# Kernel optimization log

Measured on AMD Instinct MI355X. Metric: run time of the kernel, lower is better.

The kernel has to match this reference:

```python
import jax, jax.numpy as jnp
import numpy as np

B, N, C, H, D = 1, 4096, 256, 8, 64  # batch, seq, channels, heads, head_dim


def setup_inputs() -> dict:
    key = jax.random.key(0)
    ks = jax.random.split(key, 11)
    s = 0.02
    return {
        "q_x": jax.random.normal(ks[0], (B, N, C), jnp.float32),
        "k_x": jax.random.normal(ks[1], (B, N, C), jnp.float32),
        "v_x": jax.random.normal(ks[2], (B, N, C), jnp.float32),
        "bias": jax.random.normal(ks[3], (B, 1, N, N), jnp.float32),
        "wq": jax.random.normal(ks[4], (H * D, C), jnp.float32) * s,
        "wk": jax.random.normal(ks[5], (H * D, C), jnp.float32) * s,
        "wv": jax.random.normal(ks[6], (H * D, C), jnp.float32) * s,
        "wg": jax.random.normal(ks[7], (H * D, C), jnp.float32) * s,
        "bg": jnp.ones((H * D,), jnp.float32),  # gating bias init = 1
        "wo": jax.random.normal(ks[8], (C, H * D), jnp.float32) * s,
        "bo": jnp.zeros((C,), jnp.float32),
        "q_chunk_size": 256,
        "kv_chunk_size": 1024,
    }


def reference(q_x, k_x, v_x, bias, wq, wk, wv, wg, bg, wo, bo,
              q_chunk_size, kv_chunk_size):
    # The chunked Rabe-Staats loop computes exact softmax attention; the
    # chunk sizes are memory knobs only, so the reference computes the
    # mathematically identical full attention.
    q = (q_x @ wq.T).reshape(*q_x.shape[:-1], H, D) / jnp.sqrt(jnp.asarray(D, q_x.dtype))
    k = (k_x @ wk.T).reshape(*k_x.shape[:-1], H, D)
    v = (v_x @ wv.T).reshape(*v_x.shape[:-1], H, D)
    logits = jnp.einsum("bqhd,bkhd->bhqk", q, k) + bias  # [B,H,Q,K]
    p = jax.nn.softmax(logits, axis=-1)
    o = jnp.einsum("bkhd,bhqk->bqhd", v, p)  # [B,Q,H,D]
    g = jax.nn.sigmoid(q_x @ wg.T + bg).reshape(*q_x.shape[:-1], H, D)
    o = o * g
    o = o.reshape(*o.shape[:-2], H * D)
    return o @ wo.T + bo
```

## Files before the change

kernel.cpp:

```cpp
#include <hip/hip_runtime.h>
#include <stdint.h>

#define NN 4096
#define CC 256
#define HD 512
#define DD 64
#define KSPLIT 3

typedef __attribute__((ext_vector_type(8))) short short8;
typedef __attribute__((ext_vector_type(4))) float floatx4;

__device__ __forceinline__ unsigned short f2bf(float x) {
    union { float f; unsigned int u; } v; v.f = x;
    unsigned int u = v.u + 0x7fffu + ((v.u >> 16) & 1u);
    return (unsigned short)(u >> 16);
}
__device__ __forceinline__ float bf2f(unsigned short s) {
    union { unsigned int u; float f; } v; v.u = ((unsigned int)s) << 16;
    return v.f;
}

#if defined(__has_builtin) && __has_builtin(__builtin_amdgcn_cvt_pk_bf16_f32)
typedef __attribute__((ext_vector_type(2))) __bf16 bf16x2_t;
__device__ __forceinline__ unsigned int pack2bf(float a, float b) {
    union { bf16x2_t v; unsigned int u; } x;
    x.v = __builtin_amdgcn_cvt_pk_bf16_f32(a, b);
    return x.u;
}
#else
__device__ __forceinline__ unsigned int pack2bf(float a, float b) {
    return ((unsigned int)f2bf(b) << 16) | (unsigned int)f2bf(a);
}
#endif

#define GLOAD_LDS(gp, lp) __builtin_amdgcn_global_load_lds(                    \
    (__attribute__((address_space(1))) void*)(gp),                             \
    (__attribute__((address_space(3))) void*)(lp), 16, 0, 0)

__global__ __launch_bounds__(256) void prep_kernel(
    const float* __restrict__ qx, const float* __restrict__ kx,
    const float* __restrict__ vx,
    const float* __restrict__ wq, const float* __restrict__ wk,
    const float* __restrict__ wv, const float* __restrict__ wg,
    const float* __restrict__ wo,
    unsigned short* __restrict__ qxb, unsigned short* __restrict__ kxb,
    unsigned short* __restrict__ vxb, unsigned short* __restrict__ Wb,
    unsigned short* __restrict__ wob)
{
    const int z = blockIdx.y;
    const float* src; unsigned short* dst; int n; float s = 1.0f;
    switch (z) {
        case 0: src = qx; dst = qxb; n = NN * CC; break;
        case 1: src = kx; dst = kxb; n = NN * CC; break;
        case 2: src = vx; dst = vxb; n = NN * CC; break;
        case 3: src = wq; dst = Wb;               n = HD * CC; s = 0.125f; break;
        case 4: src = wk; dst = Wb + 1 * HD * CC; n = HD * CC; break;
        case 5: src = wv; dst = Wb + 2 * HD * CC; n = HD * CC; break;
        case 6: src = wg; dst = Wb + 3 * HD * CC; n = HD * CC; break;
        default: src = wo; dst = wob;             n = CC * HD; break;
    }
    int i = (blockIdx.x * 256 + threadIdx.x) * 4;
    if (i < n) {
        float4 v = *(const float4*)&src[i];
        ushort4 p;
        p.x = f2bf(v.x * s); p.y = f2bf(v.y * s);
        p.z = f2bf(v.z * s); p.w = f2bf(v.w * s);
        *(ushort4*)&dst[i] = p;
    }
}

__global__ __launch_bounds__(256, 8) void proj_kernel(
    const unsigned short* __restrict__ qxb, const unsigned short* __restrict__ kxb,
    const unsigned short* __restrict__ vxb, const unsigned short* __restrict__ Wb,
    const float* __restrict__ bg,
    unsigned short* __restrict__ Qb, unsigned short* __restrict__ Kb,
    unsigned short* __restrict__ VbT, unsigned short* __restrict__ Gb)
{
    const int m0 = blockIdx.x * 64;
    const int nb = blockIdx.y;
    const int mode = nb >> 3;
    const int subn = nb & 7;
    const int n0 = mode * HD + subn * 64;
    const unsigned short* X = (mode == 1) ? kxb : (mode == 2) ? vxb : qxb;

    const int tid = threadIdx.x;
    const int wid = tid >> 6;
    const int lane = tid & 63;
    const int quad = lane >> 4;
    const int ln = lane & 15;
    const int lnx = ln & 7;

    __shared__ __align__(16) unsigned short smem[2 * 64 * 64];
    unsigned short* Xs = smem;
    unsigned short* Ws = smem + 64 * 64;

    floatx4 acc[4] = {};

    for (int k0 = 0; k0 < CC; k0 += 64) {
        #pragma unroll
        for (int t = 0; t < 2; t++) {
            int row = wid * 16 + t * 8 + (lane >> 3);
            int c = (lane & 7) ^ (lane >> 3);
            GLOAD_LDS(&X[(size_t)(m0 + row) * CC + k0 + c * 8],
                      &Xs[(wid * 16 + t * 8) * 64]);
            GLOAD_LDS(&Wb[(size_t)(n0 + row) * CC + k0 + c * 8],
                      &Ws[(wid * 16 + t * 8) * 64]);
        }
        __syncthreads();

        #pragma unroll
        for (int ks = 0; ks < 64; ks += 32) {
            const int cb = ks >> 3;
            short8 a = *(const short8*)&Xs[(wid * 16 + ln) * 64 +
                                           (((quad ^ cb) ^ lnx) * 8)];
            #pragma unroll
            for (int n = 0; n < 4; n++) {
                short8 b = *(const short8*)&Ws[(n * 16 + ln) * 64 +
                                               (((quad ^ cb) ^ lnx) * 8)];
                acc[n] = __builtin_amdgcn_mfma_f32_16x16x32_bf16(a, b, acc[n], 0, 0, 0);
            }
        }
        __syncthreads();
    }

    if (mode != 2) {
        unsigned short* Out = (mode == 0) ? Qb : (mode == 1) ? Kb : Gb;
        #pragma unroll
        for (int n = 0; n < 4; n++) {
            int col = subn * 64 + n * 16 + ln;
            float bgv = (mode == 3) ? bg[col] : 0.0f;
            #pragma unroll
            for (int r = 0; r < 4; r++) {
                int row = m0 + wid * 16 + quad * 4 + r;
                float v = acc[n][r];
                if (mode == 3) v = 1.0f / (1.0f + __expf(-(v + bgv)));
                Out[(size_t)row * HD + col] = f2bf(v);
            }
        }
    } else {
        #pragma unroll
        for (int n = 0; n < 4; n++) {
            int cl = n * 16 + ln;
            #pragma unroll
            for (int r = 0; r < 4; r++) {
                int rl = wid * 16 + quad * 4 + r;
                smem[cl * 72 + rl] = f2bf(acc[n][r]);
            }
        }
        __syncthreads();
        #pragma unroll
        for (int it = 0; it < 2; it++) {
            int idx = it * 256 + tid;
            int c = idx >> 3, ch = idx & 7;
            short8 vv = *(const short8*)&smem[c * 72 + ch * 8];
            *(short8*)&VbT[(size_t)(subn * 64 + c) * NN + m0 + ch * 8] = vv;
        }
    }
}

__global__ __launch_bounds__(256, 6) void attn_kernel(
    const unsigned short* __restrict__ Qb, const unsigned short* __restrict__ Kb,
    const unsigned short* __restrict__ VbT,
    const float* __restrict__ bias,
    unsigned short* __restrict__ Opart, float* __restrict__ Lpart)
{
    const int h = blockIdx.y;
    const int q0 = blockIdx.x * 64;
    const int sp = blockIdx.z;
    const int tbeg = (sp * 64) / KSPLIT;
    const int tend = ((sp + 1) * 64) / KSPLIT;
    const int tid = threadIdx.x;
    const int wid = tid >> 6;
    const int lane = tid & 63;
    const int quad = lane >> 4;
    const int ln = lane & 15;
    const int lnx = ln & 7;

    __shared__ __align__(16) unsigned short Ks[64 * 64];
    __shared__ __align__(16) unsigned short Vs[64 * 64];
    __shared__ __align__(16) unsigned short Ps[64 * 72];

    const int qrow = q0 + wid * 16 + ln;
    short8 qa0 = *(const short8*)&Qb[(size_t)qrow * HD + h * DD + quad * 8];
    short8 qa1 = *(const short8*)&Qb[(size_t)qrow * HD + h * DD + 32 + quad * 8];

    floatx4 O[4] = {};
    float lsum[4] = {0.0f, 0.0f, 0.0f, 0.0f};

    for (int kt = tbeg; kt < tend; kt++) {
        const int k0 = kt * 64;
        #pragma unroll
        for (int t = 0; t < 2; t++) {
            int row = wid * 16 + t * 8 + (lane >> 3);
            int c = (lane & 7) ^ (lane >> 3);
            GLOAD_LDS(&Kb[(size_t)(k0 + row) * HD + h * DD + c * 8],
                      &Ks[(wid * 16 + t * 8) * 64]);
            GLOAD_LDS(&VbT[(size_t)(h * DD + row) * NN + k0 + c * 8],
                      &Vs[(wid * 16 + t * 8) * 64]);
        }

        float bv[4][4];
        #pragma unroll
        for (int r = 0; r < 4; r++) {
            const float* brow = &bias[(size_t)(q0 + wid * 16 + quad * 4 + r) * NN + k0];
            #pragma unroll
            for (int n = 0; n < 4; n++) bv[r][n] = brow[n * 16 + ln];
        }
        __syncthreads();

        floatx4 S[4];
        #pragma unroll
        for (int n = 0; n < 4; n++)
            S[n] = (floatx4){bv[0][n], bv[1][n], bv[2][n], bv[3][n]};
        #pragma unroll
        for (int n = 0; n < 4; n++) {
            short8 b0 = *(const short8*)&Ks[(n * 16 + ln) * 64 + ((quad ^ lnx) * 8)];
            S[n] = __builtin_amdgcn_mfma_f32_16x16x32_bf16(qa0, b0, S[n], 0, 0, 0);
            short8 b1 = *(const short8*)&Ks[(n * 16 + ln) * 64 + (((quad ^ 4) ^ lnx) * 8)];
            S[n] = __builtin_amdgcn_mfma_f32_16x16x32_bf16(qa1, b1, S[n], 0, 0, 0);
        }

        #pragma unroll
        for (int r = 0; r < 4; r++) {
            int prow = (wid * 16 + quad * 4 + r) * 72;
            #pragma unroll
            for (int n = 0; n < 4; n += 2) {
                float p0 = __expf(S[n][r]);
                float p1 = __expf(S[n + 1][r]);
                lsum[r] += p0 + p1;
                unsigned int pk = pack2bf(p0, p1);
                Ps[prow + n * 16 + ln] = (unsigned short)(pk & 0xffffu);
                Ps[prow + (n + 1) * 16 + ln] = (unsigned short)(pk >> 16);
            }
        }

        #pragma unroll
        for (int ks = 0; ks < 64; ks += 32) {
            const int cb = ks >> 3;
            short8 a = *(const short8*)&Ps[(wid * 16 + ln) * 72 + ks + quad * 8];
            #pragma unroll
            for (int nd = 0; nd < 4; nd++) {
                short8 b = *(const short8*)&Vs[(nd * 16 + ln) * 64 +
                                               (((quad ^ cb) ^ lnx) * 8)];
                O[nd] = __builtin_amdgcn_mfma_f32_16x16x32_bf16(a, b, O[nd], 0, 0, 0);
            }
        }
        __syncthreads();
    }

    #pragma unroll
    for (int r = 0; r < 4; r++) {
        #pragma unroll
        for (int off = 1; off < 16; off <<= 1)
            lsum[r] += __shfl_xor(lsum[r], off);
        int grow = q0 + wid * 16 + quad * 4 + r;
        size_t base = ((size_t)(sp * 8 + h) * NN + grow) * 64;
        #pragma unroll
        for (int nd = 0; nd < 4; nd++)
            Opart[base + nd * 16 + ln] = f2bf(O[nd][r]);
        if (ln == 0)
            Lpart[(size_t)(sp * 8 + h) * NN + grow] = lsum[r];
    }
}

__global__ __launch_bounds__(256) void combine_kernel(
    const unsigned short* __restrict__ Opart, const float* __restrict__ Lpart,
    const unsigned short* __restrict__ Gb, unsigned short* __restrict__ OGb)
{
    const int tid = threadIdx.x;
    const int d = tid & 63;
    const int flat = blockIdx.x * 4 + (tid >> 6);
    const int h = flat >> 12;
    const int q = flat & (NN - 1);

    float l = 0.0f, o = 0.0f;
    #pragma unroll
    for (int sp = 0; sp < KSPLIT; sp++) {
        size_t idx = (size_t)(sp * 8 + h) * NN + q;
        l += Lpart[idx];
        o += bf2f(Opart[idx * 64 + d]);
    }
    float inv = 1.0f / l;
    int col = h * DD + d;
    float g = bf2f(Gb[(size_t)q * HD + col]);
    OGb[(size_t)q * HD + col] = f2bf(o * inv * g);
}

__global__ __launch_bounds__(256, 2) void outproj_kernel(
    const unsigned short* __restrict__ OGb, const unsigned short* __restrict__ wob,
    const float* __restrict__ bo, float* __restrict__ out)
{
    const int m0 = blockIdx.x * 32;
    const int n0 = blockIdx.y * 64;
    const int tid = threadIdx.x;
    const int wid = tid >> 6;
    const int wr = wid >> 1, wc = wid & 1;
    const int lane = tid & 63;
    const int quad = lane >> 4;
    const int ln = lane & 15;
    const int lnx = ln & 7;

    __shared__ __align__(16) unsigned short Xs[2][32 * 64];
    __shared__ __align__(16) unsigned short Ws[2][64 * 64];

    floatx4 acc[2] = {};

    auto STAGE = [&](int k0, int bf) {
        int c = (lane & 7) ^ (lane >> 3);
        int xrow = wid * 8 + (lane >> 3);
        GLOAD_LDS(&OGb[(size_t)(m0 + xrow) * HD + k0 + c * 8],
                  &Xs[bf][(wid * 8) * 64]);
        #pragma unroll
        for (int t = 0; t < 2; t++) {
            int wrow = wid * 16 + t * 8 + (lane >> 3);
            GLOAD_LDS(&wob[(size_t)(n0 + wrow) * HD + k0 + c * 8],
                      &Ws[bf][(wid * 16 + t * 8) * 64]);
        }
    };

    STAGE(0, 0);
    __syncthreads();

    for (int it = 0; it < 8; it++) {
        const int bf = it & 1;
        if (it + 1 < 8) STAGE((it + 1) * 64, bf ^ 1);

        #pragma unroll
        for (int ks = 0; ks < 64; ks += 32) {
            const int cb = ks >> 3;
            short8 a = *(const short8*)&Xs[bf][(wr * 16 + ln) * 64 +
                                              (((quad ^ cb) ^ lnx) * 8)];
            #pragma unroll
            for (int j = 0; j < 2; j++) {
                short8 b = *(const short8*)&Ws[bf][(wc * 32 + j * 16 + ln) * 64 +
                                                   (((quad ^ cb) ^ lnx) * 8)];
                acc[j] = __builtin_amdgcn_mfma_f32_16x16x32_bf16(a, b, acc[j], 0, 0, 0);
            }
        }
        __syncthreads();
    }

    #pragma unroll
    for (int j = 0; j < 2; j++) {
        int col = n0 + wc * 32 + j * 16 + ln;
        float bov = bo[col];
        #pragma unroll
        for (int r = 0; r < 4; r++) {
            int row = m0 + wr * 16 + quad * 4 + r;
            out[(size_t)row * CC + col] = acc[j][r] + bov;
        }
    }
}

extern "C" void kernel_launch(void* const* d_in, const int* in_sizes, int n_in,
                              void* d_out, int out_size, void* d_ws, size_t ws_size,
                              hipStream_t stream) {
    const float* qx   = (const float*)d_in[0];
    const float* kx   = (const float*)d_in[1];
    const float* vx   = (const float*)d_in[2];
    const float* bias = (const float*)d_in[3];
    const float* wq   = (const float*)d_in[4];
    const float* wk   = (const float*)d_in[5];
    const float* wv   = (const float*)d_in[6];
    const float* wg   = (const float*)d_in[7];
    const float* bg   = (const float*)d_in[8];
    const float* wo   = (const float*)d_in[9];
    const float* bo   = (const float*)d_in[10];
    float* out = (float*)d_out;

    char* ws = (char*)d_ws;
    const size_t MB = (size_t)1 << 20;
    unsigned short* wob   = (unsigned short*)(ws);
    float*          Lpart = (float*)(ws + MB / 4);
    unsigned short* Qb    = (unsigned short*)(ws + 1 * MB);
    unsigned short* Kb    = (unsigned short*)(ws + 5 * MB);
    unsigned short* VbT   = (unsigned short*)(ws + 9 * MB);
    unsigned short* Gb    = (unsigned short*)(ws + 13 * MB);
    unsigned short* OGb   = (unsigned short*)(ws + 17 * MB);
    unsigned short* qxb   = (unsigned short*)(ws + 21 * MB);
    unsigned short* kxb   = (unsigned short*)(ws + 23 * MB);
    unsigned short* vxb   = (unsigned short*)(ws + 25 * MB);
    unsigned short* Wb    = (unsigned short*)(ws + 27 * MB);
    unsigned short* Opart = (unsigned short*)(ws + 21 * MB);

    prep_kernel<<<dim3(NN * CC / (256 * 4), 8), 256, 0, stream>>>(
        qx, kx, vx, wq, wk, wv, wg, wo, qxb, kxb, vxb, Wb, wob);
    proj_kernel<<<dim3(64, 32), 256, 0, stream>>>(
        qxb, kxb, vxb, Wb, bg, Qb, Kb, VbT, Gb);
    attn_kernel<<<dim3(64, 8, KSPLIT), 256, 0, stream>>>(
        Qb, Kb, VbT, bias, Opart, Lpart);
    combine_kernel<<<dim3(NN * 8 / 4), 256, 0, stream>>>(
        Opart, Lpart, Gb, OGb);
    outproj_kernel<<<dim3(128, 4), 256, 0, stream>>>(
        OGb, wob, bo, out);
}
```

Baseline: 209.7 us.

## Fuse fp32-to-bf16 conversion into projection GEMM loads and drop prep kernel

Removes the separate prep kernel that cast the inputs and weights to bf16. The projection and output-projection GEMMs now read fp32 directly, convert in registers and write the swizzled bf16 tiles into LDS. This saves one launch and a write-then-reread of the bf16 copies. In exchange the loads become synchronous register loads instead of async global-to-LDS loads, and the output projection loses its double-buffered prefetch. Weights are also re-converted by every block.

```diff
diff --git a/kernel.cpp b/kernel.cpp
--- a/kernel.cpp
+++ b/kernel.cpp
@@ -37,41 +37,11 @@
     (__attribute__((address_space(1))) void*)(gp),                             \
     (__attribute__((address_space(3))) void*)(lp), 16, 0, 0)
 
-__global__ __launch_bounds__(256) void prep_kernel(
+__global__ __launch_bounds__(256, 8) void proj_kernel(
     const float* __restrict__ qx, const float* __restrict__ kx,
     const float* __restrict__ vx,
     const float* __restrict__ wq, const float* __restrict__ wk,
     const float* __restrict__ wv, const float* __restrict__ wg,
-    const float* __restrict__ wo,
-    unsigned short* __restrict__ qxb, unsigned short* __restrict__ kxb,
-    unsigned short* __restrict__ vxb, unsigned short* __restrict__ Wb,
-    unsigned short* __restrict__ wob)
-{
-    const int z = blockIdx.y;
-    const float* src; unsigned short* dst; int n; float s = 1.0f;
-    switch (z) {
-        case 0: src = qx; dst = qxb; n = NN * CC; break;
-        case 1: src = kx; dst = kxb; n = NN * CC; break;
-        case 2: src = vx; dst = vxb; n = NN * CC; break;
-        case 3: src = wq; dst = Wb;               n = HD * CC; s = 0.125f; break;
-        case 4: src = wk; dst = Wb + 1 * HD * CC; n = HD * CC; break;
-        case 5: src = wv; dst = Wb + 2 * HD * CC; n = HD * CC; break;
-        case 6: src = wg; dst = Wb + 3 * HD * CC; n = HD * CC; break;
-        default: src = wo; dst = wob;             n = CC * HD; break;
-    }
-    int i = (blockIdx.x * 256 + threadIdx.x) * 4;
-    if (i < n) {
-        float4 v = *(const float4*)&src[i];
-        ushort4 p;
-        p.x = f2bf(v.x * s); p.y = f2bf(v.y * s);
-        p.z = f2bf(v.z * s); p.w = f2bf(v.w * s);
-        *(ushort4*)&dst[i] = p;
-    }
-}
-
-__global__ __launch_bounds__(256, 8) void proj_kernel(
-    const unsigned short* __restrict__ qxb, const unsigned short* __restrict__ kxb,
-    const unsigned short* __restrict__ vxb, const unsigned short* __restrict__ Wb,
     const float* __restrict__ bg,
     unsigned short* __restrict__ Qb, unsigned short* __restrict__ Kb,
     unsigned short* __restrict__ VbT, unsigned short* __restrict__ Gb)
@@ -80,8 +50,10 @@
     const int nb = blockIdx.y;
     const int mode = nb >> 3;
     const int subn = nb & 7;
-    const int n0 = mode * HD + subn * 64;
-    const unsigned short* X = (mode == 1) ? kxb : (mode == 2) ? vxb : qxb;
+    const float* Xf = (mode == 1) ? kx : (mode == 2) ? vx : qx;
+    const float* Wf = (mode == 0) ? wq : (mode == 1) ? wk :
+                      (mode == 2) ? wv : wg;
+    const float wscale = (mode == 0) ? 0.125f : 1.0f;
 
     const int tid = threadIdx.x;
     const int wid = tid >> 6;
@@ -101,10 +73,21 @@
         for (int t = 0; t < 2; t++) {
             int row = wid * 16 + t * 8 + (lane >> 3);
             int c = (lane & 7) ^ (lane >> 3);
-            GLOAD_LDS(&X[(size_t)(m0 + row) * CC + k0 + c * 8],
-                      &Xs[(wid * 16 + t * 8) * 64]);
-            GLOAD_LDS(&Wb[(size_t)(n0 + row) * CC + k0 + c * 8],
-                      &Ws[(wid * 16 + t * 8) * 64]);
+            const float* xp = &Xf[(size_t)(m0 + row) * CC + k0 + c * 8];
+            const float* wp = &Wf[(size_t)(subn * 64 + row) * CC + k0 + c * 8];
+            float4 x0 = *(const float4*)xp;
+            float4 x1 = *(const float4*)(xp + 4);
+            float4 w0 = *(const float4*)wp;
+            float4 w1 = *(const float4*)(wp + 4);
+            union { unsigned int u[4]; short8 s; } px, pw;
+            px.u[0] = pack2bf(x0.x, x0.y); px.u[1] = pack2bf(x0.z, x0.w);
+            px.u[2] = pack2bf(x1.x, x1.y); px.u[3] = pack2bf(x1.z, x1.w);
+            pw.u[0] = pack2bf(w0.x * wscale, w0.y * wscale);
+            pw.u[1] = pack2bf(w0.z * wscale, w0.w * wscale);
+            pw.u[2] = pack2bf(w1.x * wscale, w1.y * wscale);
+            pw.u[3] = pack2bf(w1.z * wscale, w1.w * wscale);
+            *(short8*)&Xs[(wid * 16 + t * 8) * 64 + lane * 8] = px.s;
+            *(short8*)&Ws[(wid * 16 + t * 8) * 64 + lane * 8] = pw.s;
         }
         __syncthreads();
 
@@ -287,7 +270,7 @@
 }
 
 __global__ __launch_bounds__(256, 2) void outproj_kernel(
-    const unsigned short* __restrict__ OGb, const unsigned short* __restrict__ wob,
+    const unsigned short* __restrict__ OGb, const float* __restrict__ wo,
     const float* __restrict__ bo, float* __restrict__ out)
 {
     const int m0 = blockIdx.x * 32;
@@ -300,40 +283,39 @@
     const int ln = lane & 15;
     const int lnx = ln & 7;
 
-    __shared__ __align__(16) unsigned short Xs[2][32 * 64];
-    __shared__ __align__(16) unsigned short Ws[2][64 * 64];
+    __shared__ __align__(16) unsigned short Xs[32 * 64];
+    __shared__ __align__(16) unsigned short Ws[64 * 64];
 
     floatx4 acc[2] = {};
 
-    auto STAGE = [&](int k0, int bf) {
-        int c = (lane & 7) ^ (lane >> 3);
+    for (int it = 0; it < 8; it++) {
+        const int k0 = it * 64;
+        const int c = (lane & 7) ^ (lane >> 3);
         int xrow = wid * 8 + (lane >> 3);
         GLOAD_LDS(&OGb[(size_t)(m0 + xrow) * HD + k0 + c * 8],
-                  &Xs[bf][(wid * 8) * 64]);
+                  &Xs[(wid * 8) * 64]);
         #pragma unroll
         for (int t = 0; t < 2; t++) {
             int wrow = wid * 16 + t * 8 + (lane >> 3);
-            GLOAD_LDS(&wob[(size_t)(n0 + wrow) * HD + k0 + c * 8],
-                      &Ws[bf][(wid * 16 + t * 8) * 64]);
-        }
-    };
-
-    STAGE(0, 0);
-    __syncthreads();
-
-    for (int it = 0; it < 8; it++) {
-        const int bf = it & 1;
-        if (it + 1 < 8) STAGE((it + 1) * 64, bf ^ 1);
+            const float* wp = &wo[(size_t)(n0 + wrow) * HD + k0 + c * 8];
+            float4 w0 = *(const float4*)wp;
+            float4 w1 = *(const float4*)(wp + 4);
+            union { unsigned int u[4]; short8 s; } pw;
+            pw.u[0] = pack2bf(w0.x, w0.y); pw.u[1] = pack2bf(w0.z, w0.w);
+            pw.u[2] = pack2bf(w1.x, w1.y); pw.u[3] = pack2bf(w1.z, w1.w);
+            *(short8*)&Ws[(wid * 16 + t * 8) * 64 + lane * 8] = pw.s;
+        }
+        __syncthreads();
 
         #pragma unroll
         for (int ks = 0; ks < 64; ks += 32) {
             const int cb = ks >> 3;
-            short8 a = *(const short8*)&Xs[bf][(wr * 16 + ln) * 64 +
-                                              (((quad ^ cb) ^ lnx) * 8)];
+            short8 a = *(const short8*)&Xs[(wr * 16 + ln) * 64 +
+                                           (((quad ^ cb) ^ lnx) * 8)];
             #pragma unroll
             for (int j = 0; j < 2; j++) {
-                short8 b = *(const short8*)&Ws[bf][(wc * 32 + j * 16 + ln) * 64 +
-                                                   (((quad ^ cb) ^ lnx) * 8)];
+                short8 b = *(const short8*)&Ws[(wc * 32 + j * 16 + ln) * 64 +
+                                               (((quad ^ cb) ^ lnx) * 8)];
                 acc[j] = __builtin_amdgcn_mfma_f32_16x16x32_bf16(a, b, acc[j], 0, 0, 0);
             }
         }
@@ -370,27 +352,20 @@
 
     char* ws = (char*)d_ws;
     const size_t MB = (size_t)1 << 20;
-    unsigned short* wob   = (unsigned short*)(ws);
-    float*          Lpart = (float*)(ws + MB / 4);
+    float*          Lpart = (float*)(ws);
     unsigned short* Qb    = (unsigned short*)(ws + 1 * MB);
     unsigned short* Kb    = (unsigned short*)(ws + 5 * MB);
     unsigned short* VbT   = (unsigned short*)(ws + 9 * MB);
     unsigned short* Gb    = (unsigned short*)(ws + 13 * MB);
     unsigned short* OGb   = (unsigned short*)(ws + 17 * MB);
-    unsigned short* qxb   = (unsigned short*)(ws + 21 * MB);
-    unsigned short* kxb   = (unsigned short*)(ws + 23 * MB);
-    unsigned short* vxb   = (unsigned short*)(ws + 25 * MB);
-    unsigned short* Wb    = (unsigned short*)(ws + 27 * MB);
     unsigned short* Opart = (unsigned short*)(ws + 21 * MB);
 
-    prep_kernel<<<dim3(NN * CC / (256 * 4), 8), 256, 0, stream>>>(
-        qx, kx, vx, wq, wk, wv, wg, wo, qxb, kxb, vxb, Wb, wob);
     proj_kernel<<<dim3(64, 32), 256, 0, stream>>>(
-        qxb, kxb, vxb, Wb, bg, Qb, Kb, VbT, Gb);
+        qx, kx, vx, wq, wk, wv, wg, bg, Qb, Kb, VbT, Gb);
     attn_kernel<<<dim3(64, 8, KSPLIT), 256, 0, stream>>>(
         Qb, Kb, VbT, bias, Opart, Lpart);
     combine_kernel<<<dim3(NN * 8 / 4), 256, 0, stream>>>(
         Opart, Lpart, Gb, OGb);
     outproj_kernel<<<dim3(128, 4), 256, 0, stream>>>(
-        OGb, wob, bo, out);
-}
+        OGb, wo, bo, out);
+}
```

Measured after the change: 216.8 us. 3.4% more time.
